# Performance work log

Hardware: AMD Instinct MI355X
Metric: run time of the kernel (lower is better)

Reference implementation:

```python
import jax, jax.numpy as jnp
from jax import lax
import numpy as np


def _box_sum(x, k):
    # zero-padded sliding-window sum over last two dims of [B, H, W];
    # 'SAME' padding with additive identity 0 exactly matches nn.Unfold's
    # zero padding of k//2 on each side for odd k.
    return lax.reduce_window(x, 0.0, lax.add, (1, k, k), (1, 1, 1), 'SAME')


def _local_std(x, k):
    # torch.std over the k*k patch dim is the unbiased (n-1) sample std;
    # fused one-pass form: var = (sum(x^2) - sum(x)^2/n) / (n-1)
    n = float(k * k)
    s1 = _box_sum(x, k)
    s2 = _box_sum(x * x, k)
    var = (s2 - s1 * s1 / n) / (n - 1.0)
    return jnp.sqrt(jnp.maximum(var, 0.0))


def setup_inputs() -> dict:
    key = jax.random.key(0)
    k1, k2 = jax.random.split(key)
    B, C, H, W = 8, 6, 1024, 1024
    predictions = jax.random.normal(k1, (B, C, H, W), dtype=jnp.float32)
    targets = jax.random.randint(k2, (B, H, W), 0, C, dtype=jnp.int64)
    return {"predictions": predictions, "targets": targets, "kernel_size": 5}


def reference(predictions, targets, kernel_size):
    k = int(kernel_size)
    pred_classes = jnp.argmax(predictions, axis=1).astype(jnp.float32)  # [B,H,W]
    tgt = targets.astype(jnp.float32)                                    # [B,H,W]
    pred_consistency = _local_std(pred_classes, k)
    target_consistency = _local_std(tgt, k)
    return jnp.mean((pred_consistency - target_consistency) ** 2)
```

## Files before the change

### kernel.cpp

```cpp
#include <hip/hip_runtime.h>

#define IMG_H 1024
#define IMG_W 1024
#define HW    (IMG_H * IMG_W)
#define NCLS  6
#define NBATCH 8
#define TW 64
#define TH 32
#define HXW (TW + 4)
#define HXH (TH + 4)

__global__ __launch_bounds__(256) void fused_loss_kernel(
    const float* __restrict__ pred, const int* __restrict__ tgt,
    float* __restrict__ out) {
  __shared__ uint2 halo[HXH * HXW];
  __shared__ uint2 colsum[TH * HXW];
  __shared__ float wsum[4];

  const int b   = blockIdx.z;
  const int ty0 = blockIdx.y * TH;
  const int tx0 = blockIdx.x * TW;
  const size_t ibase = (size_t)b * HW;
  const float* pbase = pred + (size_t)b * NCLS * HW;

  for (int i = threadIdx.x; i < HXH * HXW; i += 256) {
    const int hy = i / HXW;
    const int hx = i - hy * HXW;
    const int gy = ty0 + hy - 2;
    const int gx = tx0 + hx - 2;
    uint2 v = make_uint2(0u, 0u);
    if ((unsigned)gy < IMG_H && (unsigned)gx < IMG_W) {
      const size_t pi = (size_t)gy * IMG_W + gx;
      const float* p = pbase + pi;
      float best = p[0];
      unsigned c0 = 0;
#pragma unroll
      for (int c = 1; c < NCLS; ++c) {
        const float vv = p[(size_t)c * HW];
        if (vv > best) { best = vv; c0 = (unsigned)c; }
      }
      const unsigned t = (unsigned)tgt[ibase + pi];
      v.x = c0 | ((c0 * c0) << 16);
      v.y = t  | ((t * t) << 16);
    }
    halo[i] = v;
  }
  __syncthreads();

  for (int i = threadIdx.x; i < TH * HXW; i += 256) {
    uint2 s = halo[i];
#pragma unroll
    for (int dy = 1; dy < 5; ++dy) {
      const uint2 a = halo[i + dy * HXW];
      s.x += a.x;
      s.y += a.y;
    }
    colsum[i] = s;
  }
  __syncthreads();

  float acc = 0.f;
  for (int i = threadIdx.x; i < TH * TW; i += 256) {
    const int y = i >> 6;
    const int x = i & 63;
    const int ci = y * HXW + x;
    uint2 s = colsum[ci];
#pragma unroll
    for (int dx = 1; dx < 5; ++dx) {
      const uint2 a = colsum[ci + dx];
      s.x += a.x;
      s.y += a.y;
    }
    const int s1p = (int)(s.x & 0xFFFFu), s2p = (int)(s.x >> 16);
    const int s1t = (int)(s.y & 0xFFFFu), s2t = (int)(s.y >> 16);
    const float varp = (float)(25 * s2p - s1p * s1p) * (1.0f / 600.0f);
    const float vart = (float)(25 * s2t - s1t * s1t) * (1.0f / 600.0f);
    const float d = sqrtf(varp) - sqrtf(vart);
    acc += d * d;
  }

#pragma unroll
  for (int off = 32; off > 0; off >>= 1) acc += __shfl_down(acc, off, 64);
  const int lane = threadIdx.x & 63;
  const int wid  = threadIdx.x >> 6;
  if (lane == 0) wsum[wid] = acc;
  __syncthreads();
  if (threadIdx.x == 0) {
    const float t = wsum[0] + wsum[1] + wsum[2] + wsum[3];
    atomicAdd(out, t * (1.0f / 8388608.0f));
  }
}

extern "C" void kernel_launch(void* const* d_in, const int* in_sizes, int n_in,
                              void* d_out, int out_size, void* d_ws, size_t ws_size,
                              hipStream_t stream) {
  const float* pred = (const float*)d_in[0];
  const int* tgt    = (const int*)d_in[1];
  float* out = (float*)d_out;
  (void)d_ws; (void)ws_size;

  hipMemsetAsync(d_out, 0, sizeof(float), stream);

  dim3 grid(IMG_W / TW, IMG_H / TH, NBATCH);
  fused_loss_kernel<<<grid, dim3(256), 0, stream>>>(pred, tgt, out);
}
```

Measured before the change: 328.7 us.

## Vectorize halo loads with float4 and pack classes into 16-bit shared memory

Tile interior loading now uses float4 reads of the six class planes and int4 reads of targets, doing four argmaxes per thread. The edge columns are handled by a separate scalar path. The halo is stored as one packed ushort per pixel instead of a uint2, with squares computed in the column-sum pass. Launch bounds also request 6 blocks per CU. Together these aim to cut the number of global load instructions and the shared memory footprint, at the cost of extra unpacking arithmetic and a more complex, divergent edge path.

```diff
diff --git a/kernel.cpp b/kernel.cpp
--- a/kernel.cpp
+++ b/kernel.cpp
@@ -3,17 +3,19 @@
 #define IMG_H 1024
 #define IMG_W 1024
 #define HW    (IMG_H * IMG_W)
+#define HW4   (HW / 4)
 #define NCLS  6
 #define NBATCH 8
 #define TW 64
 #define TH 32
-#define HXW (TW + 4)
-#define HXH (TH + 4)
+#define HXW 68
+#define HXH 36
+#define HS  72
 
-__global__ __launch_bounds__(256) void fused_loss_kernel(
+__global__ __launch_bounds__(256, 6) void fused_loss_kernel(
     const float* __restrict__ pred, const int* __restrict__ tgt,
     float* __restrict__ out) {
-  __shared__ uint2 halo[HXH * HXW];
+  __shared__ unsigned short halo[HXH * HS];
   __shared__ uint2 colsum[TH * HXW];
   __shared__ float wsum[4];
 
@@ -23,39 +25,69 @@
   const size_t ibase = (size_t)b * HW;
   const float* pbase = pred + (size_t)b * NCLS * HW;
 
-  for (int i = threadIdx.x; i < HXH * HXW; i += 256) {
-    const int hy = i / HXW;
-    const int hx = i - hy * HXW;
-    const int gy = ty0 + hy - 2;
-    const int gx = tx0 + hx - 2;
-    uint2 v = make_uint2(0u, 0u);
+  for (int i = threadIdx.x; i < HXH * 16; i += 256) {
+    const int row = i >> 4;
+    const int g   = i & 15;
+    const int gy  = ty0 + row - 2;
+    ushort4 pk = make_ushort4(0, 0, 0, 0);
+    if ((unsigned)gy < IMG_H) {
+      const size_t pi = (size_t)gy * IMG_W + tx0 + g * 4;
+      const float4* p = (const float4*)(pbase + pi);
+      float4 best = p[0];
+      int cx = 0, cy = 0, cz = 0, cw = 0;
+#pragma unroll
+      for (int c = 1; c < NCLS; ++c) {
+        const float4 v = p[(size_t)c * HW4];
+        if (v.x > best.x) { best.x = v.x; cx = c; }
+        if (v.y > best.y) { best.y = v.y; cy = c; }
+        if (v.z > best.z) { best.z = v.z; cz = c; }
+        if (v.w > best.w) { best.w = v.w; cw = c; }
+      }
+      const int4 t4 = *(const int4*)(tgt + ibase + pi);
+      pk.x = (unsigned short)(cx | (t4.x << 8));
+      pk.y = (unsigned short)(cy | (t4.y << 8));
+      pk.z = (unsigned short)(cz | (t4.z << 8));
+      pk.w = (unsigned short)(cw | (t4.w << 8));
+    }
+    *(ushort4*)&halo[row * HS + 4 + g * 4] = pk;
+  }
+
+  if (threadIdx.x < HXH * 4) {
+    const int row = threadIdx.x >> 2;
+    const int e   = threadIdx.x & 3;
+    const int gx  = tx0 + ((e < 2) ? (e - 2) : (62 + e));
+    const int hcol = (e < 2) ? (2 + e) : (66 + e);
+    const int gy  = ty0 + row - 2;
+    unsigned short pk = 0;
     if ((unsigned)gy < IMG_H && (unsigned)gx < IMG_W) {
       const size_t pi = (size_t)gy * IMG_W + gx;
       const float* p = pbase + pi;
       float best = p[0];
-      unsigned c0 = 0;
+      int c0 = 0;
 #pragma unroll
       for (int c = 1; c < NCLS; ++c) {
-        const float vv = p[(size_t)c * HW];
-        if (vv > best) { best = vv; c0 = (unsigned)c; }
+        const float v = p[(size_t)c * HW];
+        if (v > best) { best = v; c0 = c; }
       }
-      const unsigned t = (unsigned)tgt[ibase + pi];
-      v.x = c0 | ((c0 * c0) << 16);
-      v.y = t  | ((t * t) << 16);
+      pk = (unsigned short)(c0 | (tgt[ibase + pi] << 8));
     }
-    halo[i] = v;
+    halo[row * HS + hcol] = pk;
   }
   __syncthreads();
 
   for (int i = threadIdx.x; i < TH * HXW; i += 256) {
-    uint2 s = halo[i];
+    const int y = i / HXW;
+    const int x = i - y * HXW;
+    const unsigned short* h = &halo[y * HS + 2 + x];
+    unsigned s1p = 0, s2p = 0, s1t = 0, s2t = 0;
 #pragma unroll
-    for (int dy = 1; dy < 5; ++dy) {
-      const uint2 a = halo[i + dy * HXW];
-      s.x += a.x;
-      s.y += a.y;
+    for (int dy = 0; dy < 5; ++dy) {
+      const unsigned v = h[dy * HS];
+      const unsigned pv = v & 0xFFu, tv = v >> 8;
+      s1p += pv; s2p += pv * pv;
+      s1t += tv; s2t += tv * tv;
     }
-    colsum[i] = s;
+    colsum[i] = make_uint2(s1p | (s2p << 16), s1t | (s2t << 16));
   }
   __syncthreads();
 
```

Measured after the change: 316.1 us. -3.8%, faster.

## Use full-width row strips with float4 loads and packed byte box sums

Applied to the files above, without the earlier changes.

Each block now covers a full-width strip of 8 rows. The old design used 64x32 tiles with 2-pixel halos on all sides, so the horizontal halo is gone and the vertical halo is only 4 rows. Predictions and targets are read with float4/int4 vector loads, and argmax and target values are packed into bytes so four pixels fit in one 32-bit LDS word. Vertical and horizontal box sums are done on 8-bit packed fields, and blocks are remapped to interleave images. The goal is less redundant global traffic and halo recompute, plus wider memory transactions. In exchange the vertical halo overhead per tile grows (12/8 versus 36/32 rows) and more bit-manipulation ALU work is added.

```diff
diff --git a/kernel.cpp b/kernel.cpp
--- a/kernel.cpp
+++ b/kernel.cpp
@@ -3,89 +3,128 @@
 #define IMG_H 1024
 #define IMG_W 1024
 #define HW    (IMG_H * IMG_W)
+#define HW4   (HW / 4)
 #define NCLS  6
 #define NBATCH 8
-#define TW 64
-#define TH 32
-#define HXW (TW + 4)
-#define HXH (TH + 4)
+#define TH 8
+#define HR 12
+#define CSW 1032
 
-__global__ __launch_bounds__(256) void fused_loss_kernel(
+__global__ __launch_bounds__(256, 4) void fused_loss_kernel(
     const float* __restrict__ pred, const int* __restrict__ tgt,
     float* __restrict__ out) {
-  __shared__ uint2 halo[HXH * HXW];
-  __shared__ uint2 colsum[TH * HXW];
+  __shared__ unsigned int halo32[HR * 256];
+  __shared__ unsigned int colsum[4 * CSW];
   __shared__ float wsum[4];
 
-  const int b   = blockIdx.z;
-  const int ty0 = blockIdx.y * TH;
-  const int tx0 = blockIdx.x * TW;
-  const size_t ibase = (size_t)b * HW;
-  const float* pbase = pred + (size_t)b * NCLS * HW;
+  const int tid = threadIdx.x;
+  const int job = (blockIdx.x & 7) * 128 + (blockIdx.x >> 3);
+  const int img = job >> 7;
+  const int y0  = (job & 127) * TH;
+  const float* pimg = pred + (size_t)img * NCLS * HW;
+  const int*   timg = tgt  + (size_t)img * HW;
 
-  for (int i = threadIdx.x; i < HXH * HXW; i += 256) {
-    const int hy = i / HXW;
-    const int hx = i - hy * HXW;
-    const int gy = ty0 + hy - 2;
-    const int gx = tx0 + hx - 2;
-    uint2 v = make_uint2(0u, 0u);
-    if ((unsigned)gy < IMG_H && (unsigned)gx < IMG_W) {
-      const size_t pi = (size_t)gy * IMG_W + gx;
-      const float* p = pbase + pi;
-      float best = p[0];
-      unsigned c0 = 0;
+  if (tid < 32) {
+    const int r = tid >> 3, j = tid & 7;
+    colsum[r * CSW + ((j < 4) ? j : 1024 + j)] = 0u;
+  }
+
+  for (int k = 0; k < HR * 256; k += 256) {
+    const int id  = k + tid;
+    const int row = id >> 8;
+    const int g   = id & 255;
+    const int gy  = y0 + row - 2;
+    unsigned int w = 0u;
+    if ((unsigned)gy < IMG_H) {
+      const float4* p = (const float4*)(pimg + (size_t)gy * IMG_W) + g;
+      float4 best = p[0];
+      int cx = 0, cy = 0, cz = 0, cw = 0;
 #pragma unroll
       for (int c = 1; c < NCLS; ++c) {
-        const float vv = p[(size_t)c * HW];
-        if (vv > best) { best = vv; c0 = (unsigned)c; }
+        const float4 v = p[(size_t)c * HW4];
+        if (v.x > best.x) { best.x = v.x; cx = c; }
+        if (v.y > best.y) { best.y = v.y; cy = c; }
+        if (v.z > best.z) { best.z = v.z; cz = c; }
+        if (v.w > best.w) { best.w = v.w; cw = c; }
       }
-      const unsigned t = (unsigned)tgt[ibase + pi];
-      v.x = c0 | ((c0 * c0) << 16);
-      v.y = t  | ((t * t) << 16);
+      const int4 t4 = *((const int4*)(timg + (size_t)gy * IMG_W) + g);
+      w = (unsigned)(cx | (t4.x << 3))
+        | ((unsigned)(cy | (t4.y << 3)) << 8)
+        | ((unsigned)(cz | (t4.z << 3)) << 16)
+        | ((unsigned)(cw | (t4.w << 3)) << 24);
     }
-    halo[i] = v;
-  }
-  __syncthreads();
-
-  for (int i = threadIdx.x; i < TH * HXW; i += 256) {
-    uint2 s = halo[i];
-#pragma unroll
-    for (int dy = 1; dy < 5; ++dy) {
-      const uint2 a = halo[i + dy * HXW];
-      s.x += a.x;
-      s.y += a.y;
-    }
-    colsum[i] = s;
+    halo32[row * 256 + g] = w;
   }
   __syncthreads();
 
   float acc = 0.f;
-  for (int i = threadIdx.x; i < TH * TW; i += 256) {
-    const int y = i >> 6;
-    const int x = i & 63;
-    const int ci = y * HXW + x;
-    uint2 s = colsum[ci];
 #pragma unroll
-    for (int dx = 1; dx < 5; ++dx) {
-      const uint2 a = colsum[ci + dx];
-      s.x += a.x;
-      s.y += a.y;
+  for (int bb = 0; bb < 2; ++bb) {
+    for (int k = 0; k < 4 * 256; k += 256) {
+      const int id = k + tid;
+      const int r  = id >> 8;
+      const int g  = id & 255;
+      const unsigned int* h = &halo32[(bb * 4 + r) * 256 + g];
+      unsigned s1p[4] = {0,0,0,0}, s2p[4] = {0,0,0,0};
+      unsigned s1t[4] = {0,0,0,0}, s2t[4] = {0,0,0,0};
+#pragma unroll
+      for (int d = 0; d < 5; ++d) {
+        const unsigned wv = h[d * 256];
+#pragma unroll
+        for (int j = 0; j < 4; ++j) {
+          const unsigned pv = (wv >> (8 * j)) & 7u;
+          const unsigned tv = (wv >> (8 * j + 3)) & 7u;
+          s1p[j] += pv; s2p[j] += pv * pv;
+          s1t[j] += tv; s2t[j] += tv * tv;
+        }
+      }
+      uint4 o;
+      o.x = s1p[0] | (s2p[0] << 8) | (s1t[0] << 16) | (s2t[0] << 24);
+      o.y = s1p[1] | (s2p[1] << 8) | (s1t[1] << 16) | (s2t[1] << 24);
+      o.z = s1p[2] | (s2p[2] << 8) | (s1t[2] << 16) | (s2t[2] << 24);
+      o.w = s1p[3] | (s2p[3] << 8) | (s1t[3] << 16) | (s2t[3] << 24);
+      *(uint4*)&colsum[r * CSW + 4 + 4 * g] = o;
     }
-    const int s1p = (int)(s.x & 0xFFFFu), s2p = (int)(s.x >> 16);
-    const int s1t = (int)(s.y & 0xFFFFu), s2t = (int)(s.y >> 16);
-    const float varp = (float)(25 * s2p - s1p * s1p) * (1.0f / 600.0f);
-    const float vart = (float)(25 * s2t - s1t * s1t) * (1.0f / 600.0f);
-    const float d = sqrtf(varp) - sqrtf(vart);
-    acc += d * d;
+    __syncthreads();
+
+    for (int k = 0; k < 4 * 256; k += 256) {
+      const int id = k + tid;
+      const int r  = id >> 8;
+      const int g  = id & 255;
+      const unsigned int* cs = &colsum[r * CSW + 4 * g];
+      const uint4 wa = *(const uint4*)(cs);
+      const uint4 wb = *(const uint4*)(cs + 4);
+      const uint4 wc = *(const uint4*)(cs + 8);
+      const unsigned w[12] = {wa.x, wa.y, wa.z, wa.w,
+                              wb.x, wb.y, wb.z, wb.w,
+                              wc.x, wc.y, wc.z, wc.w};
+#pragma unroll
+      for (int j = 0; j < 4; ++j) {
+        int s1p = 0, s2p = 0, s1t = 0, s2t = 0;
+#pragma unroll
+        for (int d = 0; d < 5; ++d) {
+          const unsigned v = w[j + 2 + d];
+          s1p += (int)(v & 0xFFu);
+          s2p += (int)((v >> 8) & 0xFFu);
+          s1t += (int)((v >> 16) & 0xFFu);
+          s2t += (int)(v >> 24);
+        }
+        const float varp = (float)(25 * s2p - s1p * s1p) * (1.0f / 600.0f);
+        const float vart = (float)(25 * s2t - s1t * s1t) * (1.0f / 600.0f);
+        const float dd = sqrtf(varp) - sqrtf(vart);
+        acc += dd * dd;
+      }
+    }
+    __syncthreads();
   }
 
 #pragma unroll
   for (int off = 32; off > 0; off >>= 1) acc += __shfl_down(acc, off, 64);
-  const int lane = threadIdx.x & 63;
-  const int wid  = threadIdx.x >> 6;
+  const int lane = tid & 63;
+  const int wid  = tid >> 6;
   if (lane == 0) wsum[wid] = acc;
   __syncthreads();
-  if (threadIdx.x == 0) {
+  if (tid == 0) {
     const float t = wsum[0] + wsum[1] + wsum[2] + wsum[3];
     atomicAdd(out, t * (1.0f / 8388608.0f));
   }
@@ -101,6 +140,5 @@
 
   hipMemsetAsync(d_out, 0, sizeof(float), stream);
 
-  dim3 grid(IMG_W / TW, IMG_H / TH, NBATCH);
-  fused_loss_kernel<<<grid, dim3(256), 0, stream>>>(pred, tgt, out);
+  fused_loss_kernel<<<dim3(1024), dim3(256), 0, stream>>>(pred, tgt, out);
 }
```

Result: no change. 330.4 us (+0.5%).
